# Kernel optimization log

Hardware: AMD Instinct MI355X
Metric: run time of the kernel (lower is better)

Reference implementation:

```python
import jax, jax.numpy as jnp
import numpy as np

TOPOLOGY = [-1, 0, 0, 0, 1, 2, 3, 4, 5, 6, 7, 8, 9, 9, 9, 12, 13, 14, 16, 17, 18, 19, 20, 21]
JOINT_WEIGHTS = np.ones(24, dtype=np.float32)
B1 = 1.0
B2 = 1.0


def quaternion_to_matrix(q):
    # pytorch3d convention: real part first (w, x, y, z)
    w, x, y, z = q[..., 0], q[..., 1], q[..., 2], q[..., 3]
    two_s = 2.0 / jnp.sum(q * q, axis=-1)
    o = jnp.stack([
        1 - two_s * (y * y + z * z), two_s * (x * y - z * w), two_s * (x * z + y * w),
        two_s * (x * y + z * w), 1 - two_s * (x * x + z * z), two_s * (y * z - x * w),
        two_s * (x * z - y * w), two_s * (y * z + x * w), 1 - two_s * (x * x + y * y),
    ], axis=-1)
    return o.reshape(q.shape[:-1] + (3, 3))


def fk(topology, X_m, X_t):
    # X_m: (bs, T, J*4+3), X_t: (bs, J, 3)
    J = len(topology)
    quat = X_m[..., :-3].reshape(X_m.shape[:-1] + (J, 4))
    local_rot = quaternion_to_matrix(quat)          # (bs, T, J, 3, 3)
    grots = [None] * J
    gtrs = [None] * J
    grots[0] = local_rot[..., 0, :, :]
    gtrs[0] = X_m[..., -3:]                          # root translation
    for i in range(1, J):
        pi = topology[i]
        grots[i] = jnp.matmul(grots[pi], local_rot[..., i, :, :])
        gtrs[i] = jnp.einsum('btij,bj->bti', grots[pi], X_t[:, i]) + gtrs[pi]
    return jnp.stack(grots, axis=-3), jnp.stack(gtrs, axis=-2)


def split_raw_motion(raw_motion):
    position = raw_motion[..., -3:]
    rotation = raw_motion[..., :-3]
    rotation = rotation.reshape(rotation.shape[:-1] + (-1, 4))
    norm = jnp.linalg.norm(rotation, axis=-1, keepdims=True)
    rotation = rotation / jnp.maximum(norm, 1e-12)
    return rotation, position


def weighted_mse(w, a, b):
    # w: (J,), a/b: (bs, T, J, C) -> per-joint weighted mean squared error
    return jnp.mean(w[None, None, :, None] * (a - b) ** 2)


def setup_inputs() -> dict:
    key = jax.random.key(0)
    k1, k2, k3, k4 = jax.random.split(key, 4)
    bs, T, J = 64, 2048, 24
    return {
        'Y_m': jax.random.normal(k1, (bs, T, J * 4 + 3), dtype=jnp.float32),
        'X_m': jax.random.normal(k2, (bs, T, J * 4 + 3), dtype=jnp.float32),
        'Y_t': jax.random.normal(k3, (bs, J, 3), dtype=jnp.float32),
        'X_t': jax.random.normal(k4, (bs, J, 3), dtype=jnp.float32),
    }


def reference(Y_m, X_m, Y_t, X_t):
    w = jnp.asarray(JOINT_WEIGHTS)
    rot_x, pos_x = split_raw_motion(X_m)
    rot_y, pos_y = split_raw_motion(Y_m)
    grot_y, gtr_y = fk(TOPOLOGY, Y_m, Y_t)
    grot_x, gtr_x = fk(TOPOLOGY, X_m, X_t)
    loss_rot = B1 * weighted_mse(w, rot_y, rot_x)
    loss_fk = B2 * (2.5 * weighted_mse(w, gtr_y, gtr_x)
                    + jnp.mean((pos_y - pos_x) ** 2))
    return loss_rot + loss_fk
```

## Files before the change

kernel.cpp:

```cpp
#include <hip/hip_runtime.h>

#define NJ 24
#define ROWF 99
#define BS 64
#define TT 2048
#define NROWS (BS * TT)
#define BLOCK 256
#define NTHREADS (2 * NROWS)

typedef float f4_t __attribute__((ext_vector_type(4)));
typedef f4_t float4u __attribute__((aligned(4)));

__device__ __forceinline__ void quat2mat(float w, float x, float y, float z, float* R) {
  float s = 2.0f / (w*w + x*x + y*y + z*z);
  float xx = s*x*x, yy = s*y*y, zz = s*z*z;
  float xy = s*x*y, xz = s*x*z, yz = s*y*z;
  float xw = s*x*w, yw = s*y*w, zw = s*z*w;
  R[0] = 1.0f - (yy+zz); R[1] = xy - zw;        R[2] = xz + yw;
  R[3] = xy + zw;        R[4] = 1.0f - (xx+zz); R[5] = yz - xw;
  R[6] = xz - yw;        R[7] = yz + xw;        R[8] = 1.0f - (xx+yy);
}

__device__ __forceinline__ void mm3(const float* A, const float* B, float* C) {
#pragma unroll
  for (int r = 0; r < 3; ++r)
#pragma unroll
    for (int c = 0; c < 3; ++c)
      C[3*r+c] = fmaf(A[3*r], B[c], fmaf(A[3*r+1], B[3+c], A[3*r+2]*B[6+c]));
}

#define QMSE(q) ({ \
  float _n  = sqrtf((q).x*(q).x + (q).y*(q).y + (q).z*(q).z + (q).w*(q).w); \
  float _iv = 1.0f / fmaxf(_n, 1e-12f); \
  float _a0 = (q).x*_iv, _a1 = (q).y*_iv, _a2 = (q).z*_iv, _a3 = (q).w*_iv; \
  float _d0 = _a0 - __shfl_xor(_a0, 1, 64); \
  float _d1 = _a1 - __shfl_xor(_a1, 1, 64); \
  float _d2 = _a2 - __shfl_xor(_a2, 1, 64); \
  float _d3 = _a3 - __shfl_xor(_a3, 1, 64); \
  _d0*_d0 + _d1*_d1 + _d2*_d2 + _d3*_d3; })

#define TDIFF(t0, t1, t2) ({ \
  float _e0 = (t0) - __shfl_xor((t0), 1, 64); \
  float _e1 = (t1) - __shfl_xor((t1), 1, 64); \
  float _e2 = (t2) - __shfl_xor((t2), 1, 64); \
  _e0*_e0 + _e1*_e1 + _e2*_e2; })

#define STEP(c, GP, TP, GO, TO) do { \
  float4u q = *(const float4u*)(rowp + 4*(c)); \
  rot_acc += QMSE(q); \
  float R[9]; quat2mat(q.x, q.y, q.z, q.w, R); \
  mm3(GP, R, GO); \
  float v0 = tv[3*(c)], v1 = tv[3*(c)+1], v2 = tv[3*(c)+2]; \
  TO[0] = fmaf(GP[0], v0, fmaf(GP[1], v1, fmaf(GP[2], v2, TP[0]))); \
  TO[1] = fmaf(GP[3], v0, fmaf(GP[4], v1, fmaf(GP[5], v2, TP[1]))); \
  TO[2] = fmaf(GP[6], v0, fmaf(GP[7], v1, fmaf(GP[8], v2, TP[2]))); \
  gacc += TDIFF(TO[0], TO[1], TO[2]); \
} while (0)

#define LEAF(c, GP, TP) do { \
  float4u q = *(const float4u*)(rowp + 4*(c)); \
  rot_acc += QMSE(q); \
  float v0 = tv[3*(c)], v1 = tv[3*(c)+1], v2 = tv[3*(c)+2]; \
  float t0 = fmaf(GP[0], v0, fmaf(GP[1], v1, fmaf(GP[2], v2, TP[0]))); \
  float t1 = fmaf(GP[3], v0, fmaf(GP[4], v1, fmaf(GP[5], v2, TP[1]))); \
  float t2 = fmaf(GP[6], v0, fmaf(GP[7], v1, fmaf(GP[8], v2, TP[2]))); \
  gacc += TDIFF(t0, t1, t2); \
} while (0)

__global__ __launch_bounds__(BLOCK, 4) void motion_loss_kernel(
    const float* __restrict__ Ym, const float* __restrict__ Xm,
    const float* __restrict__ Yt, const float* __restrict__ Xt,
    float* __restrict__ out) {
  const int gtid = blockIdx.x * BLOCK + threadIdx.x;
  const int r   = gtid >> 1;
  const int par = gtid & 1;
  const float* __restrict__ rowp = (par ? Ym : Xm) + (size_t)r * ROWF;
  const int b = r >> 11;
  const float* __restrict__ tv = (par ? Yt : Xt) + (size_t)b * NJ * 3;

  float rot_acc = 0.0f, gacc = 0.0f;
  float GA[9], GB[9], GC[9], GD[9];
  float TA[3], TB[3], TC[3], TD[3];

  float4u q0 = *(const float4u*)(rowp);
  rot_acc += QMSE(q0);
  quat2mat(q0.x, q0.y, q0.z, q0.w, GA);
  TA[0] = rowp[96]; TA[1] = rowp[97]; TA[2] = rowp[98];
  float rootd2 = TDIFF(TA[0], TA[1], TA[2]);
  gacc += rootd2;

  STEP(1,  GA, TA, GB, TB);
  STEP(2,  GA, TA, GC, TC);
  STEP(3,  GA, TA, GD, TD);
  STEP(4,  GB, TB, GA, TA);
  STEP(5,  GC, TC, GB, TB);
  STEP(6,  GD, TD, GC, TC);
  STEP(7,  GA, TA, GD, TD);
  STEP(8,  GB, TB, GA, TA);
  STEP(9,  GC, TC, GB, TB);
  LEAF(10, GD, TD);
  LEAF(11, GA, TA);
  STEP(12, GB, TB, GC, TC);
  STEP(13, GB, TB, GD, TD);
  STEP(14, GB, TB, GA, TA);
  LEAF(15, GC, TC);
  STEP(16, GD, TD, GB, TB);
  STEP(17, GA, TA, GC, TC);
  STEP(18, GB, TB, GD, TD);
  STEP(19, GC, TC, GA, TA);
  STEP(20, GD, TD, GB, TB);
  STEP(21, GA, TA, GC, TC);
  LEAF(22, GB, TB);
  LEAF(23, GC, TC);

  const float c_rot = 1.0f / ((float)NROWS * NJ * 4);
  const float c_gtr = 2.5f / ((float)NROWS * NJ * 3);
  const float c_pos = 1.0f / ((float)NROWS * 3);
  float contrib = 0.5f * (c_rot * rot_acc + c_gtr * gacc + c_pos * rootd2);
#pragma unroll
  for (int o = 32; o > 0; o >>= 1) contrib += __shfl_down(contrib, o, 64);
  if ((threadIdx.x & 63) == 0) atomicAdd(out, contrib);
}

extern "C" void kernel_launch(void* const* d_in, const int* in_sizes, int n_in,
                              void* d_out, int out_size, void* d_ws, size_t ws_size,
                              hipStream_t stream) {
  const float* Ym = (const float*)d_in[0];
  const float* Xm = (const float*)d_in[1];
  const float* Yt = (const float*)d_in[2];
  const float* Xt = (const float*)d_in[3];
  float* out = (float*)d_out;
  hipMemsetAsync(out, 0, sizeof(float), stream);
  motion_loss_kernel<<<NTHREADS / BLOCK, BLOCK, 0, stream>>>(Ym, Xm, Yt, Xt, out);
}
```

Before: 186.5 us.

## Split FK chain across two lanes and stage rows through LDS with coalesced loads

Each row is now handled by four lanes (X/Y times two tree segments) instead of two. Each segment lane computes relative transforms for half the joints, and the results are then composed across lanes with a shuffle. This halves the serial per-thread dependency chain and raises parallelism. Rows are first loaded into shared memory with coalesced float4 global loads, replacing strided per-thread loads. In exchange it uses about 50KB of LDS per block, adds a tail composition pass, and lowers launch bounds occupancy to 3.

```diff
diff --git a/kernel.cpp b/kernel.cpp
--- a/kernel.cpp
+++ b/kernel.cpp
@@ -5,11 +5,15 @@
 #define BS 64
 #define TT 2048
 #define NROWS (BS * TT)
+#define TROWS 64
 #define BLOCK 256
-#define NTHREADS (2 * NROWS)
-
-typedef float f4_t __attribute__((ext_vector_type(4)));
-typedef f4_t float4u __attribute__((aligned(4)));
+#define NBLOCKS (NROWS / TROWS)
+
+#define M_FRESH 0
+#define M_NORM  1
+#define M_LEAF  2
+#define M_RSTA  3
+#define M_RSTB  4
 
 __device__ __forceinline__ void quat2mat(float w, float x, float y, float z, float* R) {
   float s = 2.0f / (w*w + x*x + y*y + z*z);
@@ -29,97 +33,168 @@
       C[3*r+c] = fmaf(A[3*r], B[c], fmaf(A[3*r+1], B[3+c], A[3*r+2]*B[6+c]));
 }
 
-#define QMSE(q) ({ \
-  float _n  = sqrtf((q).x*(q).x + (q).y*(q).y + (q).z*(q).z + (q).w*(q).w); \
-  float _iv = 1.0f / fmaxf(_n, 1e-12f); \
-  float _a0 = (q).x*_iv, _a1 = (q).y*_iv, _a2 = (q).z*_iv, _a3 = (q).w*_iv; \
-  float _d0 = _a0 - __shfl_xor(_a0, 1, 64); \
-  float _d1 = _a1 - __shfl_xor(_a1, 1, 64); \
-  float _d2 = _a2 - __shfl_xor(_a2, 1, 64); \
-  float _d3 = _a3 - __shfl_xor(_a3, 1, 64); \
-  _d0*_d0 + _d1*_d1 + _d2*_d2 + _d3*_d3; })
-
-#define TDIFF(t0, t1, t2) ({ \
-  float _e0 = (t0) - __shfl_xor((t0), 1, 64); \
-  float _e1 = (t1) - __shfl_xor((t1), 1, 64); \
-  float _e2 = (t2) - __shfl_xor((t2), 1, 64); \
-  _e0*_e0 + _e1*_e1 + _e2*_e2; })
-
-#define STEP(c, GP, TP, GO, TO) do { \
-  float4u q = *(const float4u*)(rowp + 4*(c)); \
-  rot_acc += QMSE(q); \
-  float R[9]; quat2mat(q.x, q.y, q.z, q.w, R); \
-  mm3(GP, R, GO); \
-  float v0 = tv[3*(c)], v1 = tv[3*(c)+1], v2 = tv[3*(c)+2]; \
-  TO[0] = fmaf(GP[0], v0, fmaf(GP[1], v1, fmaf(GP[2], v2, TP[0]))); \
-  TO[1] = fmaf(GP[3], v0, fmaf(GP[4], v1, fmaf(GP[5], v2, TP[1]))); \
-  TO[2] = fmaf(GP[6], v0, fmaf(GP[7], v1, fmaf(GP[8], v2, TP[2]))); \
-  gacc += TDIFF(TO[0], TO[1], TO[2]); \
+#define SCAN_STEP(S, CA, CB, MODE) do {                                        \
+  const int c_ = seg ? (CB) : (CA);                                            \
+  const float* qp_ = rowp + 4*c_;                                              \
+  float q0_ = qp_[0], q1_ = qp_[1], q2_ = qp_[2], q3_ = qp_[3];                \
+  { float n_  = sqrtf(q0_*q0_ + q1_*q1_ + q2_*q2_ + q3_*q3_);                  \
+    float iv_ = 1.0f / fmaxf(n_, 1e-12f);                                      \
+    float a0_ = q0_*iv_, a1_ = q1_*iv_, a2_ = q2_*iv_, a3_ = q3_*iv_;          \
+    float d0_ = a0_ - __shfl_xor(a0_, 1, 64);                                  \
+    float d1_ = a1_ - __shfl_xor(a1_, 1, 64);                                  \
+    float d2_ = a2_ - __shfl_xor(a2_, 1, 64);                                  \
+    float d3_ = a3_ - __shfl_xor(a3_, 1, 64);                                  \
+    rot_acc += d0_*d0_ + d1_*d1_ + d2_*d2_ + d3_*d3_; }                        \
+  float R_[9]; quat2mat(q0_, q1_, q2_, q3_, R_);                               \
+  const float* vp_ = ((S) == 0) ? vbase0 : (tvp + 3*c_);                       \
+  float v0_ = vp_[0], v1_ = vp_[1], v2_ = vp_[2];                              \
+  if ((MODE) == M_FRESH) {                                                     \
+    _Pragma("unroll") for (int i_ = 0; i_ < 9; ++i_) G[i_] = R_[i_];           \
+    T0 = v0_; T1 = v1_; T2 = v2_;                                              \
+  } else {                                                                     \
+    float Tn0_ = fmaf(G[0], v0_, fmaf(G[1], v1_, fmaf(G[2], v2_, T0)));        \
+    float Tn1_ = fmaf(G[3], v0_, fmaf(G[4], v1_, fmaf(G[5], v2_, T1)));        \
+    float Tn2_ = fmaf(G[6], v0_, fmaf(G[7], v1_, fmaf(G[8], v2_, T2)));        \
+    if ((MODE) == M_LEAF) { T0 = Tn0_; T1 = Tn1_; T2 = Tn2_; }                 \
+    else {                                                                     \
+      float Gn_[9]; mm3(G, R_, Gn_);                                           \
+      if ((MODE) == M_NORM) {                                                  \
+        _Pragma("unroll") for (int i_ = 0; i_ < 9; ++i_) G[i_] = Gn_[i_];      \
+        T0 = Tn0_; T1 = Tn1_; T2 = Tn2_;                                       \
+      } else {                                                                 \
+        bool rst_ = ((MODE) == M_RSTA) ? (seg == 0) : (seg == 1);              \
+        _Pragma("unroll") for (int i_ = 0; i_ < 9; ++i_)                       \
+          G[i_] = rst_ ? R_[i_] : Gn_[i_];                                     \
+        T0 = rst_ ? v0_ : Tn0_; T1 = rst_ ? v1_ : Tn1_; T2 = rst_ ? v2_ : Tn2_;\
+      }                                                                        \
+    }                                                                          \
+  }                                                                            \
+  trel[S][0] = T0; trel[S][1] = T1; trel[S][2] = T2;                           \
 } while (0)
 
-#define LEAF(c, GP, TP) do { \
-  float4u q = *(const float4u*)(rowp + 4*(c)); \
-  rot_acc += QMSE(q); \
-  float v0 = tv[3*(c)], v1 = tv[3*(c)+1], v2 = tv[3*(c)+2]; \
-  float t0 = fmaf(GP[0], v0, fmaf(GP[1], v1, fmaf(GP[2], v2, TP[0]))); \
-  float t1 = fmaf(GP[3], v0, fmaf(GP[4], v1, fmaf(GP[5], v2, TP[1]))); \
-  float t2 = fmaf(GP[6], v0, fmaf(GP[7], v1, fmaf(GP[8], v2, TP[2]))); \
-  gacc += TDIFF(t0, t1, t2); \
+#define TAIL_STEP(S, AG, AT) do {                                              \
+  float g0_ = fmaf(AG[0], trel[S][0], fmaf(AG[1], trel[S][1],                  \
+              fmaf(AG[2], trel[S][2], AT[0])));                                \
+  float g1_ = fmaf(AG[3], trel[S][0], fmaf(AG[4], trel[S][1],                  \
+              fmaf(AG[5], trel[S][2], AT[1])));                                \
+  float g2_ = fmaf(AG[6], trel[S][0], fmaf(AG[7], trel[S][1],                  \
+              fmaf(AG[8], trel[S][2], AT[2])));                                \
+  float e0_ = g0_ - __shfl_xor(g0_, 1, 64);                                    \
+  float e1_ = g1_ - __shfl_xor(g1_, 1, 64);                                    \
+  float e2_ = g2_ - __shfl_xor(g2_, 1, 64);                                    \
+  float d2_ = e0_*e0_ + e1_*e1_ + e2_*e2_;                                     \
+  gacc += d2_;                                                                 \
+  if ((S) == 0) pos_d2 = d2_;                                                  \
 } while (0)
 
-__global__ __launch_bounds__(BLOCK, 4) void motion_loss_kernel(
+__global__ __launch_bounds__(BLOCK, 3) void motion_loss_kernel(
     const float* __restrict__ Ym, const float* __restrict__ Xm,
     const float* __restrict__ Yt, const float* __restrict__ Xt,
     float* __restrict__ out) {
-  const int gtid = blockIdx.x * BLOCK + threadIdx.x;
-  const int r   = gtid >> 1;
-  const int par = gtid & 1;
-  const float* __restrict__ rowp = (par ? Ym : Xm) + (size_t)r * ROWF;
-  const int b = r >> 11;
-  const float* __restrict__ tv = (par ? Yt : Xt) + (size_t)b * NJ * 3;
-
-  float rot_acc = 0.0f, gacc = 0.0f;
-  float GA[9], GB[9], GC[9], GD[9];
-  float TA[3], TB[3], TC[3], TD[3];
-
-  float4u q0 = *(const float4u*)(rowp);
-  rot_acc += QMSE(q0);
-  quat2mat(q0.x, q0.y, q0.z, q0.w, GA);
-  TA[0] = rowp[96]; TA[1] = rowp[97]; TA[2] = rowp[98];
-  float rootd2 = TDIFF(TA[0], TA[1], TA[2]);
-  gacc += rootd2;
-
-  STEP(1,  GA, TA, GB, TB);
-  STEP(2,  GA, TA, GC, TC);
-  STEP(3,  GA, TA, GD, TD);
-  STEP(4,  GB, TB, GA, TA);
-  STEP(5,  GC, TC, GB, TB);
-  STEP(6,  GD, TD, GC, TC);
-  STEP(7,  GA, TA, GD, TD);
-  STEP(8,  GB, TB, GA, TA);
-  STEP(9,  GC, TC, GB, TB);
-  LEAF(10, GD, TD);
-  LEAF(11, GA, TA);
-  STEP(12, GB, TB, GC, TC);
-  STEP(13, GB, TB, GD, TD);
-  STEP(14, GB, TB, GA, TA);
-  LEAF(15, GC, TC);
-  STEP(16, GD, TD, GB, TB);
-  STEP(17, GA, TA, GC, TC);
-  STEP(18, GB, TB, GD, TD);
-  STEP(19, GC, TC, GA, TA);
-  STEP(20, GD, TD, GB, TB);
-  STEP(21, GA, TA, GC, TC);
-  LEAF(22, GB, TB);
-  LEAF(23, GC, TC);
+  __shared__ __align__(16) float tileX[TROWS * ROWF];
+  __shared__ __align__(16) float tileY[TROWS * ROWF];
+  __shared__ float tvX[NJ * 3], tvY[NJ * 3];
+
+  const int tid = threadIdx.x;
+  const int blk = blockIdx.x;
+  const size_t row0 = (size_t)blk * TROWS;
+  const int b = (int)(row0 >> 11);
+
+  const float4* gx = (const float4*)(Xm + row0 * ROWF);
+  const float4* gy = (const float4*)(Ym + row0 * ROWF);
+  float4 rx[6], ry[6];
+  float4 rtx = {0,0,0,0}, rty = {0,0,0,0};
+#pragma unroll
+  for (int k = 0; k < 6; ++k) rx[k] = gx[k * BLOCK + tid];
+#pragma unroll
+  for (int k = 0; k < 6; ++k) ry[k] = gy[k * BLOCK + tid];
+  const bool tail48 = (tid < (TROWS * ROWF / 4 - 6 * BLOCK));
+  if (tail48) { rtx = gx[6 * BLOCK + tid]; rty = gy[6 * BLOCK + tid]; }
+  float tvv = 0.0f;
+  if (tid < 72) tvv = Xt[(size_t)b * 72 + tid];
+  else if (tid < 144) tvv = Yt[(size_t)b * 72 + (tid - 72)];
+
+  float4* lx4 = (float4*)tileX;
+  float4* ly4 = (float4*)tileY;
+#pragma unroll
+  for (int k = 0; k < 6; ++k) lx4[k * BLOCK + tid] = rx[k];
+#pragma unroll
+  for (int k = 0; k < 6; ++k) ly4[k * BLOCK + tid] = ry[k];
+  if (tail48) { lx4[6 * BLOCK + tid] = rtx; ly4[6 * BLOCK + tid] = rty; }
+  if (tid < 72) tvX[tid] = tvv;
+  else if (tid < 144) tvY[tid - 72] = tvv;
+  __syncthreads();
+
+  const int par = tid & 1;
+  const int seg = (tid >> 1) & 1;
+  const int rl  = tid >> 2;
+  const float* __restrict__ rowp = (par ? tileY : tileX) + rl * ROWF;
+  const float* __restrict__ tvp  = par ? tvY : tvX;
+  const float* vbase0 = seg ? (tvp + 3 * 13) : (rowp + 96);
+
+  float rot_acc = 0.0f, gacc = 0.0f, pos_d2 = 0.0f;
+  float G[9], T0, T1, T2;
+  float trel[12][3];
+
+  SCAN_STEP(0,  0, 13, M_FRESH);
+  float A0G[9], A0T[3];
+#pragma unroll
+  for (int i = 0; i < 9; ++i) A0G[i] = G[i];
+  A0T[0] = T0; A0T[1] = T1; A0T[2] = T2;
+  SCAN_STEP(1,  1, 16, M_NORM);
+  SCAN_STEP(2,  4, 18, M_NORM);
+  SCAN_STEP(3,  7, 20, M_NORM);
+  SCAN_STEP(4, 10, 22, M_LEAF);
+  SCAN_STEP(5,  2, 14, M_FRESH);
+  SCAN_STEP(6,  5, 17, M_NORM);
+  SCAN_STEP(7,  8, 19, M_NORM);
+  SCAN_STEP(8, 11, 21, M_NORM);
+  SCAN_STEP(9,  3, 23, M_RSTA);
+  SCAN_STEP(10, 6, 12, M_RSTB);
+  SCAN_STEP(11, 9, 15, M_NORM);
+
+  float A9G[9], A9T[3];
+  mm3(A0G, G, A9G);
+  A9T[0] = fmaf(A0G[0], T0, fmaf(A0G[1], T1, fmaf(A0G[2], T2, A0T[0])));
+  A9T[1] = fmaf(A0G[3], T0, fmaf(A0G[4], T1, fmaf(A0G[5], T2, A0T[1])));
+  A9T[2] = fmaf(A0G[6], T0, fmaf(A0G[7], T1, fmaf(A0G[8], T2, A0T[2])));
+
+  float A1G[9], A1T[3], A2G[9], A2T[3];
+#pragma unroll
+  for (int i = 0; i < 9; ++i) {
+    float r = __shfl_xor(A9G[i], 2, 64);
+    float idv = (i == 0 || i == 4 || i == 8) ? 1.0f : 0.0f;
+    A2G[i] = seg ? r : A0G[i];
+    A1G[i] = seg ? r : idv;
+  }
+#pragma unroll
+  for (int i = 0; i < 3; ++i) {
+    float r = __shfl_xor(A9T[i], 2, 64);
+    A2T[i] = seg ? r : A0T[i];
+    A1T[i] = seg ? r : 0.0f;
+  }
+
+  TAIL_STEP(0,  A1G, A1T);
+  TAIL_STEP(1,  A1G, A1T);
+  TAIL_STEP(2,  A1G, A1T);
+  TAIL_STEP(3,  A1G, A1T);
+  TAIL_STEP(4,  A1G, A1T);
+  TAIL_STEP(5,  A2G, A2T);
+  TAIL_STEP(6,  A2G, A2T);
+  TAIL_STEP(7,  A2G, A2T);
+  TAIL_STEP(8,  A2G, A2T);
+  TAIL_STEP(9,  A2G, A2T);
+  TAIL_STEP(10, A2G, A2T);
+  TAIL_STEP(11, A2G, A2T);
 
   const float c_rot = 1.0f / ((float)NROWS * NJ * 4);
   const float c_gtr = 2.5f / ((float)NROWS * NJ * 3);
   const float c_pos = 1.0f / ((float)NROWS * 3);
-  float contrib = 0.5f * (c_rot * rot_acc + c_gtr * gacc + c_pos * rootd2);
+  float posw = seg ? 0.0f : 1.0f;
+  float contrib = 0.5f * (c_rot * rot_acc + c_gtr * gacc + c_pos * pos_d2 * posw);
 #pragma unroll
   for (int o = 32; o > 0; o >>= 1) contrib += __shfl_down(contrib, o, 64);
-  if ((threadIdx.x & 63) == 0) atomicAdd(out, contrib);
+  if ((tid & 63) == 0) atomicAdd(out, contrib);
 }
 
 extern "C" void kernel_launch(void* const* d_in, const int* in_sizes, int n_in,
@@ -131,5 +206,5 @@
   const float* Xt = (const float*)d_in[3];
   float* out = (float*)d_out;
   hipMemsetAsync(out, 0, sizeof(float), stream);
-  motion_loss_kernel<<<NTHREADS / BLOCK, BLOCK, 0, stream>>>(Ym, Xm, Yt, Xt, out);
-}
+  motion_loss_kernel<<<NBLOCKS, BLOCK, 0, stream>>>(Ym, Xm, Yt, Xt, out);
+}
```

Result: slower. 216.6 us (+16.1%).

## Stage row tiles through LDS with coalesced float4 loads before per-row FK

Applied to the files above, without the earlier changes.

Each 64-thread block now cooperatively copies 32 contiguous rows of X_m and Y_m into shared memory using coalesced float4 loads, plus the per-batch offset vectors. Threads then read their row's quaternions from LDS instead of doing strided per-thread global loads. This replaces uncoalesced 99-float-stride accesses with fully coalesced streaming. The cost is ~25KB of LDS per block and a barrier, which lowers occupancy, and many more blocks each do an atomicAdd.

```diff
diff --git a/kernel.cpp b/kernel.cpp
--- a/kernel.cpp
+++ b/kernel.cpp
@@ -5,11 +5,10 @@
 #define BS 64
 #define TT 2048
 #define NROWS (BS * TT)
-#define BLOCK 256
-#define NTHREADS (2 * NROWS)
-
-typedef float f4_t __attribute__((ext_vector_type(4)));
-typedef f4_t float4u __attribute__((aligned(4)));
+#define TROWS 32
+#define BLOCK 64
+#define NBLOCKS (NROWS / TROWS)
+#define TILE4 (TROWS * ROWF / 4)
 
 __device__ __forceinline__ void quat2mat(float w, float x, float y, float z, float* R) {
   float s = 2.0f / (w*w + x*x + y*y + z*z);
@@ -29,10 +28,10 @@
       C[3*r+c] = fmaf(A[3*r], B[c], fmaf(A[3*r+1], B[3+c], A[3*r+2]*B[6+c]));
 }
 
-#define QMSE(q) ({ \
-  float _n  = sqrtf((q).x*(q).x + (q).y*(q).y + (q).z*(q).z + (q).w*(q).w); \
+#define QMSE(q0, q1, q2, q3) ({ \
+  float _n  = sqrtf((q0)*(q0) + (q1)*(q1) + (q2)*(q2) + (q3)*(q3)); \
   float _iv = 1.0f / fmaxf(_n, 1e-12f); \
-  float _a0 = (q).x*_iv, _a1 = (q).y*_iv, _a2 = (q).z*_iv, _a3 = (q).w*_iv; \
+  float _a0 = (q0)*_iv, _a1 = (q1)*_iv, _a2 = (q2)*_iv, _a3 = (q3)*_iv; \
   float _d0 = _a0 - __shfl_xor(_a0, 1, 64); \
   float _d1 = _a1 - __shfl_xor(_a1, 1, 64); \
   float _d2 = _a2 - __shfl_xor(_a2, 1, 64); \
@@ -46,9 +45,9 @@
   _e0*_e0 + _e1*_e1 + _e2*_e2; })
 
 #define STEP(c, GP, TP, GO, TO) do { \
-  float4u q = *(const float4u*)(rowp + 4*(c)); \
-  rot_acc += QMSE(q); \
-  float R[9]; quat2mat(q.x, q.y, q.z, q.w, R); \
+  float q0 = rowp[4*(c)], q1 = rowp[4*(c)+1], q2 = rowp[4*(c)+2], q3 = rowp[4*(c)+3]; \
+  rot_acc += QMSE(q0, q1, q2, q3); \
+  float R[9]; quat2mat(q0, q1, q2, q3, R); \
   mm3(GP, R, GO); \
   float v0 = tv[3*(c)], v1 = tv[3*(c)+1], v2 = tv[3*(c)+2]; \
   TO[0] = fmaf(GP[0], v0, fmaf(GP[1], v1, fmaf(GP[2], v2, TP[0]))); \
@@ -58,8 +57,8 @@
 } while (0)
 
 #define LEAF(c, GP, TP) do { \
-  float4u q = *(const float4u*)(rowp + 4*(c)); \
-  rot_acc += QMSE(q); \
+  float q0 = rowp[4*(c)], q1 = rowp[4*(c)+1], q2 = rowp[4*(c)+2], q3 = rowp[4*(c)+3]; \
+  rot_acc += QMSE(q0, q1, q2, q3); \
   float v0 = tv[3*(c)], v1 = tv[3*(c)+1], v2 = tv[3*(c)+2]; \
   float t0 = fmaf(GP[0], v0, fmaf(GP[1], v1, fmaf(GP[2], v2, TP[0]))); \
   float t1 = fmaf(GP[3], v0, fmaf(GP[4], v1, fmaf(GP[5], v2, TP[1]))); \
@@ -67,24 +66,68 @@
   gacc += TDIFF(t0, t1, t2); \
 } while (0)
 
-__global__ __launch_bounds__(BLOCK, 4) void motion_loss_kernel(
+__global__ __launch_bounds__(BLOCK, 2) void motion_loss_kernel(
     const float* __restrict__ Ym, const float* __restrict__ Xm,
     const float* __restrict__ Yt, const float* __restrict__ Xt,
     float* __restrict__ out) {
-  const int gtid = blockIdx.x * BLOCK + threadIdx.x;
-  const int r   = gtid >> 1;
-  const int par = gtid & 1;
-  const float* __restrict__ rowp = (par ? Ym : Xm) + (size_t)r * ROWF;
-  const int b = r >> 11;
-  const float* __restrict__ tv = (par ? Yt : Xt) + (size_t)b * NJ * 3;
+  __shared__ __align__(16) float tX[TROWS * ROWF];
+  __shared__ __align__(16) float tY[TROWS * ROWF];
+  __shared__ float tvX[NJ * 3], tvY[NJ * 3];
+
+  const int lane = threadIdx.x;
+  const int blk = blockIdx.x;
+  const size_t row0 = (size_t)blk * TROWS;
+  const int b = (int)(row0 >> 11);
+
+  const float4* gx = (const float4*)(Xm + row0 * ROWF);
+  const float4* gy = (const float4*)(Ym + row0 * ROWF);
+  float4* lx4 = (float4*)tX;
+  float4* ly4 = (float4*)tY;
+  {
+    float4 r0[6], r1[6];
+#pragma unroll
+    for (int k = 0; k < 6; ++k) r0[k] = gx[k * BLOCK + lane];
+#pragma unroll
+    for (int k = 0; k < 6; ++k) r1[k] = gy[k * BLOCK + lane];
+#pragma unroll
+    for (int k = 0; k < 6; ++k) lx4[k * BLOCK + lane] = r0[k];
+#pragma unroll
+    for (int k = 0; k < 6; ++k) ly4[k * BLOCK + lane] = r1[k];
+#pragma unroll
+    for (int k = 0; k < 6; ++k) r0[k] = gx[(6 + k) * BLOCK + lane];
+#pragma unroll
+    for (int k = 0; k < 6; ++k) r1[k] = gy[(6 + k) * BLOCK + lane];
+#pragma unroll
+    for (int k = 0; k < 6; ++k) lx4[(6 + k) * BLOCK + lane] = r0[k];
+#pragma unroll
+    for (int k = 0; k < 6; ++k) ly4[(6 + k) * BLOCK + lane] = r1[k];
+    if (lane < TILE4 - 12 * BLOCK) {
+      lx4[12 * BLOCK + lane] = gx[12 * BLOCK + lane];
+      ly4[12 * BLOCK + lane] = gy[12 * BLOCK + lane];
+    }
+  }
+#pragma unroll
+  for (int k = 0; k < 3; ++k) {
+    int id = k * BLOCK + lane;
+    if (id < 72) tvX[id] = Xt[(size_t)b * 72 + id];
+    else if (id < 144) tvY[id - 72] = Yt[(size_t)b * 72 + (id - 72)];
+  }
+  __syncthreads();
+
+  const int par = lane & 1;
+  const int rl  = lane >> 1;
+  const float* __restrict__ rowp = (par ? tY : tX) + rl * ROWF;
+  const float* __restrict__ tv   = par ? tvY : tvX;
 
   float rot_acc = 0.0f, gacc = 0.0f;
   float GA[9], GB[9], GC[9], GD[9];
   float TA[3], TB[3], TC[3], TD[3];
 
-  float4u q0 = *(const float4u*)(rowp);
-  rot_acc += QMSE(q0);
-  quat2mat(q0.x, q0.y, q0.z, q0.w, GA);
+  {
+    float q0 = rowp[0], q1 = rowp[1], q2 = rowp[2], q3 = rowp[3];
+    rot_acc += QMSE(q0, q1, q2, q3);
+    quat2mat(q0, q1, q2, q3, GA);
+  }
   TA[0] = rowp[96]; TA[1] = rowp[97]; TA[2] = rowp[98];
   float rootd2 = TDIFF(TA[0], TA[1], TA[2]);
   gacc += rootd2;
@@ -119,7 +162,7 @@
   float contrib = 0.5f * (c_rot * rot_acc + c_gtr * gacc + c_pos * rootd2);
 #pragma unroll
   for (int o = 32; o > 0; o >>= 1) contrib += __shfl_down(contrib, o, 64);
-  if ((threadIdx.x & 63) == 0) atomicAdd(out, contrib);
+  if (lane == 0) atomicAdd(out, contrib);
 }
 
 extern "C" void kernel_launch(void* const* d_in, const int* in_sizes, int n_in,
@@ -131,5 +174,5 @@
   const float* Xt = (const float*)d_in[3];
   float* out = (float*)d_out;
   hipMemsetAsync(out, 0, sizeof(float), stream);
-  motion_loss_kernel<<<NTHREADS / BLOCK, BLOCK, 0, stream>>>(Ym, Xm, Yt, Xt, out);
+  motion_loss_kernel<<<NBLOCKS, BLOCK, 0, stream>>>(Ym, Xm, Yt, Xt, out);
 }
```

New measurement: 175.9 us. 1.06x faster.
